# Performance work log

Hardware: AMD Instinct MI355X
Metric: run time of the kernel (lower is better)

The kernel has to match this reference:

```python
import jax, jax.numpy as jnp
import numpy as np

N, H, HD = 512, 8, 128          # n_nodes, n_heads, h feature dim
M0, M1 = 256, 256               # mlp_units
NORM_CONST = 1.0


def setup_inputs() -> dict:
    key = jax.random.key(0)
    ks = jax.random.split(key, 16)
    def w(k, i, o, scale=1.0):
        return jax.random.normal(k, (i, o), jnp.float32) * (scale / np.sqrt(i))
    F = HD + H * H               # h_concat dim = 128 + 64 = 192
    EIN = H + 2 * F              # edge MLP input dim = 8 + 384 = 392
    return {
        "x": jax.random.normal(ks[0], (N, H, 3), jnp.float32),
        "h": jax.random.normal(ks[1], (N, HD), jnp.float32),
        # phi_e: MLP([256,256], silu, activate_final=True)
        "We0": w(ks[2], EIN, M0), "be0": jnp.zeros((M0,), jnp.float32),
        "We1": w(ks[3], M0, M1), "be1": jnp.zeros((M1,), jnp.float32),
        # phi_inf: Linear(1) + sigmoid
        "Winf": w(ks[4], M1, 1), "binf": jnp.zeros((1,), jnp.float32),
        # phi_x: MLP([256,256], silu, activate_final=True) -> Linear(n_heads) (variance-scaled small init)
        "Wx0": w(ks[5], M1, M0), "bx0": jnp.zeros((M0,), jnp.float32),
        "Wx1": w(ks[6], M0, M1), "bx1": jnp.zeros((M1,), jnp.float32),
        "Wxo": w(ks[7], M1, H, scale=0.03), "bxo": jnp.zeros((H,), jnp.float32),
        # phi_h: MLP([256,256], silu, activate_final=False)... note haiku MLP applies
        # activation between layers; final Linear(h_dim) appended in forward.
        "Wh0": w(ks[8], M1 + HD, M0), "bh0": jnp.zeros((M0,), jnp.float32),
        "Wh1": w(ks[9], M0, M1), "bh1": jnp.zeros((M1,), jnp.float32),
        "Who": w(ks[10], M1, HD), "bho": jnp.zeros((HD,), jnp.float32),
    }


def _forward(x, h, We0, be0, We1, be1, Winf, binf, Wx0, bx0, Wx1, bx1,
             Wxo, bxo, Wh0, bh0, Wh1, bh1, Who, bho):
    n, nh = x.shape[0], x.shape[1]
    silu = jax.nn.silu
    off = 1.0 - jnp.eye(n, dtype=x.dtype)                  # off-diagonal node mask
    # per-node head-pair squared distances -> [N, H*H] (diag naturally 0)
    dh = x[:, :, None, :] - x[:, None, :, :]               # [N,H,H,3]
    sqh = jnp.sum(dh * dh, axis=-1).reshape(n, nh * nh)
    hc = jnp.concatenate([h, sqh], axis=-1)                # [N, F]
    # all-pairs node diffs per head: dn[i,j,h] = x[j,h] - x[i,h]
    dn = x[None] - x[:, None]                              # [N,N,H,3]
    sqn = jnp.sum(dn * dn, axis=-1)                        # [N,N,H]
    F = hc.shape[-1]
    hc_j = jnp.broadcast_to(hc[None], (n, n, F))           # receiver-side: hc[j]
    hc_i = jnp.broadcast_to(hc[:, None], (n, n, F))        # sender-side: hc[i]
    edge_in = jnp.concatenate([sqn, hc_j, hc_i], axis=-1)  # [N,N,H+2F]
    # phi_e (activate_final=True), zero self-edges
    m = silu(silu(edge_in @ We0 + be0) @ We1 + be1) * off[:, :, None]
    # gate + message aggregation
    e = jax.nn.sigmoid(m @ Winf + binf)[..., 0] * off      # [N,N]
    m_i = jnp.einsum('ijd,ij->id', m, e)                   # [N,M1]
    # phi_x multi-head coordinate weights (tanh=False), zero self-edges
    px = (silu(silu(m @ Wx0 + bx0) @ Wx1 + bx1) @ Wxo + bxo) * off[:, :, None]
    # normalize_by_x_norm=True path
    norm = jnp.sqrt(sqn + 1e-8) + NORM_CONST               # [N,N,H]
    ndiff = (dn / norm[..., None]) * off[:, :, None, None]
    shift = jnp.einsum('ijhd,ijh->ihd', ndiff, px) / (n - 1)  # agg='mean'
    x_new = x + shift
    # phi_h with residual
    ph_in = jnp.concatenate([m_i, h], axis=-1)
    h_new = h + silu(silu(ph_in @ Wh0 + bh0) @ Wh1 + bh1) @ Who + bho
    return x_new, h_new


def reference(x, h, We0, be0, We1, be1, Winf, binf, Wx0, bx0, Wx1, bx1,
              Wxo, bxo, Wh0, bh0, Wh1, bh1, Who, bho):
    return _forward(x, h, We0, be0, We1, be1, Winf, binf, Wx0, bx0, Wx1, bx1,
                    Wxo, bxo, Wh0, bh0, Wh1, bh1, Who, bho)
```

## Files before the change

kernel.cpp:

```cpp
#include <hip/hip_runtime.h>
#include <math.h>

#define N_NODES 512
#define NH 8
#define HD 128
#define M 256
#define PITCH 264
#define JTILE 64
#define RPW 16

typedef __bf16 v8bf __attribute__((ext_vector_type(8)));
typedef float f32x4 __attribute__((ext_vector_type(4)));
typedef unsigned short us4v __attribute__((ext_vector_type(4)));

__device__ __forceinline__ float silu_f(float v) {
  return v * __builtin_amdgcn_rcpf(1.f + __expf(-v));
}
__device__ __forceinline__ float sigmoid_f(float v) {
  return __builtin_amdgcn_rcpf(1.f + __expf(-v));
}
__device__ __forceinline__ unsigned short f2bf(float f) {
  unsigned u = __float_as_uint(f);
  u += 0x7fffu + ((u >> 16) & 1u);
  return (unsigned short)(u >> 16);
}
__device__ __forceinline__ unsigned short f2bf_hi(float f) {
  return (unsigned short)((__float_as_uint(f) + 0x8000u) >> 16);
}
__device__ __forceinline__ float bf2f(unsigned short s) {
  return __uint_as_float(((unsigned)s) << 16);
}

__device__ __forceinline__ void gl2lds16(const unsigned short* g, unsigned short* l) {
  __builtin_amdgcn_global_load_lds(
      (const __attribute__((address_space(1))) unsigned int*)g,
      (__attribute__((address_space(3))) unsigned int*)l, 16, 0, 0);
}

__global__ __launch_bounds__(256) void k_pre(
    const float* __restrict__ x, const float* __restrict__ h,
    const float* __restrict__ We0, const float* __restrict__ be0,
    const float* __restrict__ We1, const float* __restrict__ Wx0,
    const float* __restrict__ Wx1, const float* __restrict__ Wxo,
    unsigned short* __restrict__ wsB,
    float* __restrict__ P, float* __restrict__ Q,
    float* __restrict__ mi, float* __restrict__ shift)
{
  const int t = threadIdx.x;
  if (blockIdx.x < 816) {
    const int gid = blockIdx.x * 256 + t;
    if (gid >= 208896) return;
    float val;
    int dst;
    if (gid < 196608) {
      const int layer = gid >> 16, e = gid & 65535;
      const int k = e >> 8, n = e & 255;
      const float* W = (layer == 0) ? We1 : (layer == 1) ? Wx0 : Wx1;
      val = W[e];
      const int kt = k >> 5, w = k & 31, quad = w >> 3, j = w & 7;
      const int nt = n >> 4, lnib = n & 15;
      dst = layer * 65536 + ((kt * 16 + nt) * 64 + quad * 16 + lnib) * 8 + j;
    } else if (gid < 198656) {
      const int e = gid - 196608;
      val = Wxo[e];
      const int k = e >> 3, col = e & 7;
      const int kt = k >> 5, w = k & 31, quad = w >> 3, j = w & 7;
      dst = 196608 + (kt * 64 + quad * 16 + col) * 8 + j;
    } else if (gid < 200704) {
      const int e = gid - 198656;
      val = 0.f;
      const int k = e >> 3, col = e & 7;
      const int kt = k >> 5, w = k & 31, quad = w >> 3, j = w & 7;
      dst = 196608 + (kt * 64 + quad * 16 + col + 8) * 8 + j;
    } else if (gid < 202752) {
      const int e = gid - 200704;
      val = We0[e];
      const int j = e >> 8, n = e & 255, nt = n >> 4, lnib = n & 15;
      dst = 200704 + (nt * 64 + lnib) * 8 + j;
    } else {
      const int e = gid - 202752;
      val = 0.f;
      const int q = 1 + (e >> 11), rem = e & 2047;
      const int j = rem & 7, lnib = (rem >> 3) & 15, nt = rem >> 7;
      dst = 200704 + (nt * 64 + q * 16 + lnib) * 8 + j;
    }
    wsB[dst] = f2bf(val);
    return;
  }
  const int i = blockIdx.x - 816;
  __shared__ float s_x[24];
  __shared__ float s_hc[192];
  mi[i * M + t] = 0.f;
  if (t < 24) { shift[i * 24 + t] = 0.f; s_x[t] = x[i * 24 + t]; }
  __syncthreads();
  if (t < HD) {
    s_hc[t] = h[i * HD + t];
  } else if (t < 192) {
    const int p = t - HD, a = p >> 3, b = p & 7;
    float s = 0.f;
#pragma unroll
    for (int d = 0; d < 3; ++d) {
      const float dx = s_x[a * 3 + d] - s_x[b * 3 + d];
      s = fmaf(dx, dx, s);
    }
    s_hc[t] = s;
  }
  __syncthreads();
  float p = 0.f, q = 0.f;
  for (int k = 0; k < 192; ++k) {
    const float hv = s_hc[k];
    p = fmaf(hv, We0[(8 + k) * M + t], p);
    q = fmaf(hv, We0[(200 + k) * M + t], q);
  }
  P[i * M + t] = p;
  Q[i * M + t] = q + be0[t];
}

__global__ __launch_bounds__(512, 4) void k_edge(
    const float* __restrict__ x,
    const float* __restrict__ P, const float* __restrict__ Q,
    const float* __restrict__ be1,
    const float* __restrict__ Winf, const float* __restrict__ binf,
    const float* __restrict__ bx0, const float* __restrict__ bx1,
    const float* __restrict__ bxo,
    const unsigned short* __restrict__ wsB,
    float* __restrict__ mi_acc, float* __restrict__ shift_acc)
{
  const int i  = blockIdx.x;
  const int j0 = blockIdx.y * JTILE;
  const int t  = threadIdx.x;
  const int lane = t & 63, wave = t >> 6;
  const int lnib = lane & 15, quad = lane >> 4;
  const int rg = wave >> 1, c = wave & 1;
  const int r0 = rg * RPW;
  const int jw = j0 + r0;
  const int cb = c * 128;

  __shared__ __align__(16) unsigned short a_act[JTILE * PITCH];
  __shared__ __align__(16) unsigned short B_buf[2][8192];
  __shared__ __align__(16) float s_sqn[JTILE][8];
  __shared__ __align__(16) unsigned short s_sqnb[JTILE][8];
  __shared__ float s_red[JTILE][2];
  __shared__ float s_e[JTILE];

  auto stage = [&](const unsigned short* __restrict__ Bg, int kt, int which) {
    const unsigned short* src = Bg + kt * 8192 + wave * 1024 + lane * 8;
    unsigned short* dst = &B_buf[which][wave * 1024];
    gl2lds16(src,       dst);
    gl2lds16(src + 512, dst + 512);
  };

#pragma unroll
  for (int kk = 0; kk < 2; ++kk) {
    const int idx = kk * 64 + lane;
    const int r = idx >> 3, hh = idx & 7;
    const int j = jw + r;
    float s = 0.f;
#pragma unroll
    for (int d = 0; d < 3; ++d) {
      const float dx = x[j * 24 + hh * 3 + d] - x[i * 24 + hh * 3 + d];
      s = fmaf(dx, dx, s);
    }
    s_sqn[r0 + r][hh] = s;
    s_sqnb[r0 + r][hh] = f2bf(s);
  }

  stage(wsB, 0, 0);

  const float binf0 = binf[0];

  f32x4 acc[8];

  {
#pragma unroll
    for (int nt = 0; nt < 8; ++nt)
#pragma unroll
      for (int reg = 0; reg < 4; ++reg)
        acc[nt][reg] = P[(jw + quad * 4 + reg) * M + cb + nt * 16 + lnib];
    const v8bf aS = *(const v8bf*)&s_sqnb[r0 + lnib][0];
    const unsigned short* B0 = wsB + 200704;
#pragma unroll
    for (int nt = 0; nt < 8; ++nt) {
      const v8bf bv = *(const v8bf*)&B0[((c * 8 + nt) * 64 + lane) * 8];
      acc[nt] = __builtin_amdgcn_mfma_f32_16x16x32_bf16(aS, bv, acc[nt], 0, 0, 0);
    }
#pragma unroll
    for (int nt = 0; nt < 8; ++nt) {
      const float qv = Q[i * M + cb + nt * 16 + lnib];
#pragma unroll
      for (int reg = 0; reg < 4; ++reg) {
        const int row = r0 + quad * 4 + reg;
        a_act[row * PITCH + cb + nt * 16 + lnib] = f2bf_hi(silu_f(acc[nt][reg] + qv));
      }
    }
  }

  auto run_gemm = [&](const unsigned short* __restrict__ Bg,
                      const unsigned short* __restrict__ Bnext) {
    __syncthreads();
#pragma unroll
    for (int kt = 0; kt < 8; ++kt) {
      if (kt < 7)      stage(Bg, kt + 1, (kt + 1) & 1);
      else if (Bnext)  stage(Bnext, 0, 0);
      const v8bf a0 = *(const v8bf*)&a_act[(r0 + lnib) * PITCH + kt * 32 + quad * 8];
#pragma unroll
      for (int nt = 0; nt < 8; ++nt) {
        const v8bf bv = *(const v8bf*)&B_buf[kt & 1][(c * 8 + nt) * 512 + lane * 8];
        acc[nt] = __builtin_amdgcn_mfma_f32_16x16x32_bf16(a0, bv, acc[nt], 0, 0, 0);
      }
      __syncthreads();
    }
  };

#pragma unroll
  for (int nt = 0; nt < 8; ++nt) {
    const float b = be1[cb + nt * 16 + lnib];
    acc[nt] = (f32x4){b, b, b, b};
  }
  run_gemm(wsB, wsB + 65536);
  {
    float ge[4] = {0.f, 0.f, 0.f, 0.f};
#pragma unroll
    for (int nt = 0; nt < 8; ++nt) {
      const float wfv = Winf[cb + nt * 16 + lnib];
#pragma unroll
      for (int reg = 0; reg < 4; ++reg) {
        float v = silu_f(acc[nt][reg]);
        const int row = r0 + quad * 4 + reg;
        if (j0 + row == i) v = 0.f;
        a_act[row * PITCH + cb + nt * 16 + lnib] = f2bf_hi(v);
        ge[reg] = fmaf(v, wfv, ge[reg]);
      }
    }
#pragma unroll
    for (int reg = 0; reg < 4; ++reg) {
      float g = ge[reg];
      g += __shfl_xor(g, 1);
      g += __shfl_xor(g, 2);
      g += __shfl_xor(g, 4);
      g += __shfl_xor(g, 8);
      if (lnib == 0) s_red[r0 + quad * 4 + reg][c] = g;
    }
  }
  __syncthreads();
  if (t < JTILE) s_e[t] = sigmoid_f(s_red[t][0] + s_red[t][1] + binf0);
  __syncthreads();

  {
    const int ch = cb + lane * 2;
    float m0 = 0.f, m1 = 0.f;
#pragma unroll
    for (int r = 0; r < RPW; ++r) {
      const unsigned mv = *(const unsigned*)&a_act[(r0 + r) * PITCH + ch];
      const float ev = s_e[r0 + r];
      m0 = fmaf(bf2f((unsigned short)(mv & 0xffffu)), ev, m0);
      m1 = fmaf(bf2f((unsigned short)(mv >> 16)), ev, m1);
    }
    atomicAdd(&mi_acc[i * M + ch + 0], m0);
    atomicAdd(&mi_acc[i * M + ch + 1], m1);
  }

#pragma unroll
  for (int nt = 0; nt < 8; ++nt) {
    const float b = bx0[cb + nt * 16 + lnib];
    acc[nt] = (f32x4){b, b, b, b};
  }
  run_gemm(wsB + 65536, wsB + 131072);
#pragma unroll
  for (int nt = 0; nt < 8; ++nt)
#pragma unroll
    for (int reg = 0; reg < 4; ++reg) {
      const int row = r0 + quad * 4 + reg;
      a_act[row * PITCH + cb + nt * 16 + lnib] = f2bf_hi(silu_f(acc[nt][reg]));
    }

#pragma unroll
  for (int nt = 0; nt < 8; ++nt) {
    const float b = bx1[cb + nt * 16 + lnib];
    acc[nt] = (f32x4){b, b, b, b};
  }
  run_gemm(wsB + 131072, nullptr);
#pragma unroll
  for (int nt = 0; nt < 8; ++nt)
#pragma unroll
    for (int reg = 0; reg < 4; ++reg) {
      const int row = r0 + quad * 4 + reg;
      a_act[row * PITCH + cb + nt * 16 + lnib] = f2bf_hi(silu_f(acc[nt][reg]));
    }
  __syncthreads();

  if (c == 0) {
    f32x4 px;
    {
      const float b = (lnib < 8) ? bxo[lnib] : 0.f;
      px = (f32x4){b, b, b, b};
      const unsigned short* B = wsB + 196608;
#pragma unroll
      for (int kt = 0; kt < 8; ++kt) {
        const v8bf a0 = *(const v8bf*)&a_act[(r0 + lnib) * PITCH + kt * 32 + quad * 8];
        const v8bf bv = *(const v8bf*)&B[(kt * 64 + lane) * 8];
        px = __builtin_amdgcn_mfma_f32_16x16x32_bf16(a0, bv, px, 0, 0, 0);
      }
    }
    const int hh = lnib & 7;
    const float xi0 = x[i * 24 + hh * 3 + 0];
    const float xi1 = x[i * 24 + hh * 3 + 1];
    const float xi2 = x[i * 24 + hh * 3 + 2];
    float p0 = 0.f, p1 = 0.f, p2 = 0.f;
#pragma unroll
    for (int reg = 0; reg < 4; ++reg) {
      const int row = r0 + quad * 4 + reg;
      const int jg = j0 + row;
      if (jg != i) {
        const float pxv = px[reg];
        const float sq  = s_sqn[row][hh];
        const float f   = pxv * __builtin_amdgcn_rcpf(sqrtf(sq + 1e-8f) + 1.f);
        p0 = fmaf(x[jg * 24 + hh * 3 + 0] - xi0, f, p0);
        p1 = fmaf(x[jg * 24 + hh * 3 + 1] - xi1, f, p1);
        p2 = fmaf(x[jg * 24 + hh * 3 + 2] - xi2, f, p2);
      }
    }
    p0 += __shfl_xor(p0, 16); p0 += __shfl_xor(p0, 32);
    p1 += __shfl_xor(p1, 16); p1 += __shfl_xor(p1, 32);
    p2 += __shfl_xor(p2, 16); p2 += __shfl_xor(p2, 32);
    if (lane < 8) {
      atomicAdd(&shift_acc[i * 24 + hh * 3 + 0], p0);
      atomicAdd(&shift_acc[i * 24 + hh * 3 + 1], p1);
      atomicAdd(&shift_acc[i * 24 + hh * 3 + 2], p2);
    }
  }
}

__global__ __launch_bounds__(256) void k_hout(
    const float* __restrict__ x, const float* __restrict__ shift,
    const float* __restrict__ h, const float* __restrict__ mi,
    const float* __restrict__ Wh0, const float* __restrict__ bh0,
    const float* __restrict__ Wh1, const float* __restrict__ bh1,
    const float* __restrict__ Who, const float* __restrict__ bho,
    float* __restrict__ out_x, float* __restrict__ out_h)
{
  const int i = blockIdx.x, t = threadIdx.x;
  __shared__ float s_in[M + HD];
  __shared__ float s_b[M];
  if (t < 24) out_x[i * 24 + t] = x[i * 24 + t] + shift[i * 24 + t] * (1.f / 511.f);
  s_in[t] = mi[i * M + t];
  if (t < HD) s_in[M + t] = h[i * HD + t];
  __syncthreads();
  float acc = bh0[t];
  for (int k = 0; k < M + HD; ++k) acc = fmaf(s_in[k], Wh0[k * M + t], acc);
  s_b[t] = silu_f(acc);
  __syncthreads();
  float acc2 = bh1[t];
  for (int k = 0; k < M; ++k) acc2 = fmaf(s_b[k], Wh1[k * M + t], acc2);
  const float a1v = silu_f(acc2);
  __syncthreads();
  s_in[t] = a1v;
  __syncthreads();
  if (t < HD) {
    float o = bho[t];
    for (int k = 0; k < M; ++k) o = fmaf(s_in[k], Who[k * HD + t], o);
    out_h[i * HD + t] = h[i * HD + t] + o;
  }
}

extern "C" void kernel_launch(void* const* d_in, const int* in_sizes, int n_in,
                              void* d_out, int out_size, void* d_ws, size_t ws_size,
                              hipStream_t stream)
{
  const float* x    = (const float*)d_in[0];
  const float* h    = (const float*)d_in[1];
  const float* We0  = (const float*)d_in[2];
  const float* be0  = (const float*)d_in[3];
  const float* We1  = (const float*)d_in[4];
  const float* be1  = (const float*)d_in[5];
  const float* Winf = (const float*)d_in[6];
  const float* binf = (const float*)d_in[7];
  const float* Wx0  = (const float*)d_in[8];
  const float* bx0  = (const float*)d_in[9];
  const float* Wx1  = (const float*)d_in[10];
  const float* bx1  = (const float*)d_in[11];
  const float* Wxo  = (const float*)d_in[12];
  const float* bxo  = (const float*)d_in[13];
  const float* Wh0  = (const float*)d_in[14];
  const float* bh0  = (const float*)d_in[15];
  const float* Wh1  = (const float*)d_in[16];
  const float* bh1  = (const float*)d_in[17];
  const float* Who  = (const float*)d_in[18];
  const float* bho  = (const float*)d_in[19];

  float* out_x = (float*)d_out;
  float* out_h = out_x + N_NODES * NH * 3;

  float* ws    = (float*)d_ws;
  float* mi    = ws;
  float* shift = ws + 131072;
  float* P     = ws + 143360;
  float* Q     = ws + 274432;
  unsigned short* wsB = (unsigned short*)(ws + 405504);

  k_pre<<<816 + N_NODES, 256, 0, stream>>>(
      x, h, We0, be0, We1, Wx0, Wx1, Wxo, wsB, P, Q, mi, shift);
  k_edge<<<dim3(N_NODES, N_NODES / JTILE), 512, 0, stream>>>(
      x, P, Q, be1, Winf, binf, bx0, bx1, bxo, wsB, mi, shift);
  k_hout<<<N_NODES, 256, 0, stream>>>(
      x, shift, h, mi, Wh0, bh0, Wh1, bh1, Who, bho, out_x, out_h);
}
```

Measured before the change: 307.8 us.

## Retile edge MLP to 4 waves with 4x4 MFMA tiles and swapped operands

The edge kernel moves from 8 waves of 16 rows by 128 columns to 4 waves that each own 64 columns across all 64 edges. Each wave now runs a 4x4 grid of MFMA tiles, so every loaded A and B fragment is reused four times. Operands are swapped so each lane's accumulator holds four consecutive channels, which allows vectorized bias/P/Q loads and packed bf16 stores via v_cvt_pk_bf16. The tradeoff is higher register pressure from 16 accumulators per lane and fewer waves per block, which may lower occupancy and latency hiding.

```diff
diff --git a/kernel.cpp b/kernel.cpp
--- a/kernel.cpp
+++ b/kernel.cpp
@@ -7,11 +7,10 @@
 #define M 256
 #define PITCH 264
 #define JTILE 64
-#define RPW 16
 
 typedef __bf16 v8bf __attribute__((ext_vector_type(8)));
 typedef float f32x4 __attribute__((ext_vector_type(4)));
-typedef unsigned short us4v __attribute__((ext_vector_type(4)));
+typedef unsigned uint2v __attribute__((ext_vector_type(2)));
 
 __device__ __forceinline__ float silu_f(float v) {
   return v * __builtin_amdgcn_rcpf(1.f + __expf(-v));
@@ -24,11 +23,13 @@
   u += 0x7fffu + ((u >> 16) & 1u);
   return (unsigned short)(u >> 16);
 }
-__device__ __forceinline__ unsigned short f2bf_hi(float f) {
-  return (unsigned short)((__float_as_uint(f) + 0x8000u) >> 16);
-}
 __device__ __forceinline__ float bf2f(unsigned short s) {
   return __uint_as_float(((unsigned)s) << 16);
+}
+__device__ __forceinline__ unsigned cvt_pk_bf16(float lo, float hi) {
+  unsigned r;
+  asm("v_cvt_pk_bf16_f32 %0, %1, %2" : "=v"(r) : "v"(lo), "v"(hi));
+  return r;
 }
 
 __device__ __forceinline__ void gl2lds16(const unsigned short* g, unsigned short* l) {
@@ -116,7 +117,7 @@
   Q[i * M + t] = q + be0[t];
 }
 
-__global__ __launch_bounds__(512, 4) void k_edge(
+__global__ __launch_bounds__(256, 2) void k_edge(
     const float* __restrict__ x,
     const float* __restrict__ P, const float* __restrict__ Q,
     const float* __restrict__ be1,
@@ -129,68 +130,77 @@
   const int i  = blockIdx.x;
   const int j0 = blockIdx.y * JTILE;
   const int t  = threadIdx.x;
-  const int lane = t & 63, wave = t >> 6;
+  const int lane = t & 63, wq = t >> 6;
   const int lnib = lane & 15, quad = lane >> 4;
-  const int rg = wave >> 1, c = wave & 1;
-  const int r0 = rg * RPW;
-  const int jw = j0 + r0;
-  const int cb = c * 128;
+  const int cb = wq * 64;
 
   __shared__ __align__(16) unsigned short a_act[JTILE * PITCH];
   __shared__ __align__(16) unsigned short B_buf[2][8192];
   __shared__ __align__(16) float s_sqn[JTILE][8];
   __shared__ __align__(16) unsigned short s_sqnb[JTILE][8];
-  __shared__ float s_red[JTILE][2];
+  __shared__ float s_red[JTILE][4];
   __shared__ float s_e[JTILE];
 
   auto stage = [&](const unsigned short* __restrict__ Bg, int kt, int which) {
-    const unsigned short* src = Bg + kt * 8192 + wave * 1024 + lane * 8;
-    unsigned short* dst = &B_buf[which][wave * 1024];
-    gl2lds16(src,       dst);
-    gl2lds16(src + 512, dst + 512);
+    const unsigned short* src = Bg + kt * 8192 + wq * 2048 + lane * 8;
+    unsigned short* dst = &B_buf[which][wq * 2048];
+    gl2lds16(src,        dst);
+    gl2lds16(src + 512,  dst + 512);
+    gl2lds16(src + 1024, dst + 1024);
+    gl2lds16(src + 1536, dst + 1536);
   };
 
 #pragma unroll
   for (int kk = 0; kk < 2; ++kk) {
-    const int idx = kk * 64 + lane;
+    const int idx = kk * 256 + t;
     const int r = idx >> 3, hh = idx & 7;
-    const int j = jw + r;
+    const int j = j0 + r;
     float s = 0.f;
 #pragma unroll
     for (int d = 0; d < 3; ++d) {
       const float dx = x[j * 24 + hh * 3 + d] - x[i * 24 + hh * 3 + d];
       s = fmaf(dx, dx, s);
     }
-    s_sqn[r0 + r][hh] = s;
-    s_sqnb[r0 + r][hh] = f2bf(s);
+    s_sqn[r][hh] = s;
+    s_sqnb[r][hh] = f2bf(s);
   }
 
   stage(wsB, 0, 0);
-
   const float binf0 = binf[0];
-
-  f32x4 acc[8];
+  __syncthreads();
+
+  f32x4 acc[4][4];
 
   {
 #pragma unroll
-    for (int nt = 0; nt < 8; ++nt)
-#pragma unroll
-      for (int reg = 0; reg < 4; ++reg)
-        acc[nt][reg] = P[(jw + quad * 4 + reg) * M + cb + nt * 16 + lnib];
-    const v8bf aS = *(const v8bf*)&s_sqnb[r0 + lnib][0];
-    const unsigned short* B0 = wsB + 200704;
-#pragma unroll
-    for (int nt = 0; nt < 8; ++nt) {
-      const v8bf bv = *(const v8bf*)&B0[((c * 8 + nt) * 64 + lane) * 8];
-      acc[nt] = __builtin_amdgcn_mfma_f32_16x16x32_bf16(aS, bv, acc[nt], 0, 0, 0);
-    }
-#pragma unroll
-    for (int nt = 0; nt < 8; ++nt) {
-      const float qv = Q[i * M + cb + nt * 16 + lnib];
-#pragma unroll
-      for (int reg = 0; reg < 4; ++reg) {
-        const int row = r0 + quad * 4 + reg;
-        a_act[row * PITCH + cb + nt * 16 + lnib] = f2bf_hi(silu_f(acc[nt][reg] + qv));
+    for (int ct = 0; ct < 4; ++ct)
+#pragma unroll
+      for (int et = 0; et < 4; ++et)
+        acc[ct][et] = *(const f32x4*)&P[(j0 + et * 16 + lnib) * M + cb + ct * 16 + quad * 4];
+    const unsigned short* W0 = wsB + 200704;
+    v8bf wf[4], af[4];
+#pragma unroll
+    for (int ct = 0; ct < 4; ++ct)
+      wf[ct] = *(const v8bf*)&W0[((wq * 4 + ct) * 64 + lane) * 8];
+#pragma unroll
+    for (int et = 0; et < 4; ++et)
+      af[et] = *(const v8bf*)&s_sqnb[et * 16 + lnib][0];
+#pragma unroll
+    for (int ct = 0; ct < 4; ++ct)
+#pragma unroll
+      for (int et = 0; et < 4; ++et)
+        acc[ct][et] = __builtin_amdgcn_mfma_f32_16x16x32_bf16(wf[ct], af[et], acc[ct][et], 0, 0, 0);
+#pragma unroll
+    for (int ct = 0; ct < 4; ++ct) {
+      const f32x4 qv = *(const f32x4*)&Q[i * M + cb + ct * 16 + quad * 4];
+#pragma unroll
+      for (int et = 0; et < 4; ++et) {
+        const int row = et * 16 + lnib;
+        const unsigned w0 = cvt_pk_bf16(silu_f(acc[ct][et][0] + qv[0]),
+                                        silu_f(acc[ct][et][1] + qv[1]));
+        const unsigned w1 = cvt_pk_bf16(silu_f(acc[ct][et][2] + qv[2]),
+                                        silu_f(acc[ct][et][3] + qv[3]));
+        *(uint2v*)&a_act[row * PITCH + cb + ct * 16 + quad * 4] = (uint2v){w0, w1};
       }
     }
   }
@@ -202,131 +212,161 @@
     for (int kt = 0; kt < 8; ++kt) {
       if (kt < 7)      stage(Bg, kt + 1, (kt + 1) & 1);
       else if (Bnext)  stage(Bnext, 0, 0);
-      const v8bf a0 = *(const v8bf*)&a_act[(r0 + lnib) * PITCH + kt * 32 + quad * 8];
-#pragma unroll
-      for (int nt = 0; nt < 8; ++nt) {
-        const v8bf bv = *(const v8bf*)&B_buf[kt & 1][(c * 8 + nt) * 512 + lane * 8];
-        acc[nt] = __builtin_amdgcn_mfma_f32_16x16x32_bf16(a0, bv, acc[nt], 0, 0, 0);
-      }
+      v8bf wf[4], af[4];
+#pragma unroll
+      for (int ct = 0; ct < 4; ++ct)
+        wf[ct] = *(const v8bf*)&B_buf[kt & 1][(wq * 4 + ct) * 512 + lane * 8];
+#pragma unroll
+      for (int et = 0; et < 4; ++et)
+        af[et] = *(const v8bf*)&a_act[(et * 16 + lnib) * PITCH + kt * 32 + quad * 8];
+#pragma unroll
+      for (int ct = 0; ct < 4; ++ct)
+#pragma unroll
+        for (int et = 0; et < 4; ++et)
+          acc[ct][et] = __builtin_amdgcn_mfma_f32_16x16x32_bf16(wf[ct], af[et], acc[ct][et], 0, 0, 0);
       __syncthreads();
     }
   };
 
 #pragma unroll
-  for (int nt = 0; nt < 8; ++nt) {
-    const float b = be1[cb + nt * 16 + lnib];
-    acc[nt] = (f32x4){b, b, b, b};
+  for (int ct = 0; ct < 4; ++ct) {
+    const f32x4 b = *(const f32x4*)&be1[cb + ct * 16 + quad * 4];
+#pragma unroll
+    for (int et = 0; et < 4; ++et) acc[ct][et] = b;
   }
   run_gemm(wsB, wsB + 65536);
   {
     float ge[4] = {0.f, 0.f, 0.f, 0.f};
 #pragma unroll
-    for (int nt = 0; nt < 8; ++nt) {
-      const float wfv = Winf[cb + nt * 16 + lnib];
-#pragma unroll
-      for (int reg = 0; reg < 4; ++reg) {
-        float v = silu_f(acc[nt][reg]);
-        const int row = r0 + quad * 4 + reg;
-        if (j0 + row == i) v = 0.f;
-        a_act[row * PITCH + cb + nt * 16 + lnib] = f2bf_hi(v);
-        ge[reg] = fmaf(v, wfv, ge[reg]);
+    for (int ct = 0; ct < 4; ++ct) {
+      const f32x4 wv = *(const f32x4*)&Winf[cb + ct * 16 + quad * 4];
+#pragma unroll
+      for (int et = 0; et < 4; ++et) {
+        const int row = et * 16 + lnib;
+        const bool dz = (j0 + row == i);
+        const float v0 = dz ? 0.f : silu_f(acc[ct][et][0]);
+        const float v1 = dz ? 0.f : silu_f(acc[ct][et][1]);
+        const float v2 = dz ? 0.f : silu_f(acc[ct][et][2]);
+        const float v3 = dz ? 0.f : silu_f(acc[ct][et][3]);
+        ge[et] = fmaf(v0, wv[0], ge[et]);
+        ge[et] = fmaf(v1, wv[1], ge[et]);
+        ge[et] = fmaf(v2, wv[2], ge[et]);
+        ge[et] = fmaf(v3, wv[3], ge[et]);
+        *(uint2v*)&a_act[row * PITCH + cb + ct * 16 + quad * 4] =
+            (uint2v){cvt_pk_bf16(v0, v1), cvt_pk_bf16(v2, v3)};
       }
     }
 #pragma unroll
-    for (int reg = 0; reg < 4; ++reg) {
-      float g = ge[reg];
-      g += __shfl_xor(g, 1);
-      g += __shfl_xor(g, 2);
-      g += __shfl_xor(g, 4);
-      g += __shfl_xor(g, 8);
-      if (lnib == 0) s_red[r0 + quad * 4 + reg][c] = g;
-    }
-  }
-  __syncthreads();
-  if (t < JTILE) s_e[t] = sigmoid_f(s_red[t][0] + s_red[t][1] + binf0);
+    for (int et = 0; et < 4; ++et) {
+      float g = ge[et];
+      g += __shfl_xor(g, 16);
+      g += __shfl_xor(g, 32);
+      if (quad == 0) s_red[et * 16 + lnib][wq] = g;
+    }
+  }
+  __syncthreads();
+  if (t < JTILE)
+    s_e[t] = sigmoid_f(s_red[t][0] + s_red[t][1] + s_red[t][2] + s_red[t][3] + binf0);
   __syncthreads();
 
   {
-    const int ch = cb + lane * 2;
-    float m0 = 0.f, m1 = 0.f;
-#pragma unroll
-    for (int r = 0; r < RPW; ++r) {
-      const unsigned mv = *(const unsigned*)&a_act[(r0 + r) * PITCH + ch];
+    const int r0 = wq * 16;
+    float m0 = 0.f, m1 = 0.f, m2 = 0.f, m3 = 0.f;
+#pragma unroll
+    for (int r = 0; r < 16; ++r) {
       const float ev = s_e[r0 + r];
-      m0 = fmaf(bf2f((unsigned short)(mv & 0xffffu)), ev, m0);
-      m1 = fmaf(bf2f((unsigned short)(mv >> 16)), ev, m1);
-    }
-    atomicAdd(&mi_acc[i * M + ch + 0], m0);
-    atomicAdd(&mi_acc[i * M + ch + 1], m1);
-  }
-
-#pragma unroll
-  for (int nt = 0; nt < 8; ++nt) {
-    const float b = bx0[cb + nt * 16 + lnib];
-    acc[nt] = (f32x4){b, b, b, b};
+      const unsigned pa = *(const unsigned*)&a_act[(r0 + r) * PITCH + lane * 2];
+      const unsigned pb = *(const unsigned*)&a_act[(r0 + r) * PITCH + 128 + lane * 2];
+      m0 = fmaf(bf2f((unsigned short)(pa & 0xffffu)), ev, m0);
+      m1 = fmaf(bf2f((unsigned short)(pa >> 16)), ev, m1);
+      m2 = fmaf(bf2f((unsigned short)(pb & 0xffffu)), ev, m2);
+      m3 = fmaf(bf2f((unsigned short)(pb >> 16)), ev, m3);
+    }
+    atomicAdd(&mi_acc[i * M + lane * 2 + 0], m0);
+    atomicAdd(&mi_acc[i * M + lane * 2 + 1], m1);
+    atomicAdd(&mi_acc[i * M + 128 + lane * 2 + 0], m2);
+    atomicAdd(&mi_acc[i * M + 128 + lane * 2 + 1], m3);
+  }
+
+#pragma unroll
+  for (int ct = 0; ct < 4; ++ct) {
+    const f32x4 b = *(const f32x4*)&bx0[cb + ct * 16 + quad * 4];
+#pragma unroll
+    for (int et = 0; et < 4; ++et) acc[ct][et] = b;
   }
   run_gemm(wsB + 65536, wsB + 131072);
 #pragma unroll
-  for (int nt = 0; nt < 8; ++nt)
-#pragma unroll
-    for (int reg = 0; reg < 4; ++reg) {
-      const int row = r0 + quad * 4 + reg;
-      a_act[row * PITCH + cb + nt * 16 + lnib] = f2bf_hi(silu_f(acc[nt][reg]));
-    }
-
-#pragma unroll
-  for (int nt = 0; nt < 8; ++nt) {
-    const float b = bx1[cb + nt * 16 + lnib];
-    acc[nt] = (f32x4){b, b, b, b};
+  for (int ct = 0; ct < 4; ++ct)
+#pragma unroll
+    for (int et = 0; et < 4; ++et) {
+      const int row = et * 16 + lnib;
+      const unsigned w0 = cvt_pk_bf16(silu_f(acc[ct][et][0]), silu_f(acc[ct][et][1]));
+      const unsigned w1 = cvt_pk_bf16(silu_f(acc[ct][et][2]), silu_f(acc[ct][et][3]));
+      *(uint2v*)&a_act[row * PITCH + cb + ct * 16 + quad * 4] = (uint2v){w0, w1};
+    }
+
+#pragma unroll
+  for (int ct = 0; ct < 4; ++ct) {
+    const f32x4 b = *(const f32x4*)&bx1[cb + ct * 16 + quad * 4];
+#pragma unroll
+    for (int et = 0; et < 4; ++et) acc[ct][et] = b;
   }
   run_gemm(wsB + 131072, nullptr);
 #pragma unroll
-  for (int nt = 0; nt < 8; ++nt)
-#pragma unroll
-    for (int reg = 0; reg < 4; ++reg) {
-      const int row = r0 + quad * 4 + reg;
-      a_act[row * PITCH + cb + nt * 16 + lnib] = f2bf_hi(silu_f(acc[nt][reg]));
-    }
-  __syncthreads();
-
-  if (c == 0) {
+  for (int ct = 0; ct < 4; ++ct)
+#pragma unroll
+    for (int et = 0; et < 4; ++et) {
+      const int row = et * 16 + lnib;
+      const unsigned w0 = cvt_pk_bf16(silu_f(acc[ct][et][0]), silu_f(acc[ct][et][1]));
+      const unsigned w1 = cvt_pk_bf16(silu_f(acc[ct][et][2]), silu_f(acc[ct][et][3]));
+      *(uint2v*)&a_act[row * PITCH + cb + ct * 16 + quad * 4] = (uint2v){w0, w1};
+    }
+  __syncthreads();
+
+  {
+    const int e0 = wq * 16;
     f32x4 px;
-    {
-      const float b = (lnib < 8) ? bxo[lnib] : 0.f;
-      px = (f32x4){b, b, b, b};
-      const unsigned short* B = wsB + 196608;
-#pragma unroll
-      for (int kt = 0; kt < 8; ++kt) {
-        const v8bf a0 = *(const v8bf*)&a_act[(r0 + lnib) * PITCH + kt * 32 + quad * 8];
-        const v8bf bv = *(const v8bf*)&B[(kt * 64 + lane) * 8];
-        px = __builtin_amdgcn_mfma_f32_16x16x32_bf16(a0, bv, px, 0, 0, 0);
+    if (quad < 2) px = *(const f32x4*)&bxo[quad * 4];
+    else          px = (f32x4){0.f, 0.f, 0.f, 0.f};
+    const unsigned short* Bx = wsB + 196608;
+#pragma unroll
+    for (int kt = 0; kt < 8; ++kt) {
+      const v8bf af = *(const v8bf*)&a_act[(e0 + lnib) * PITCH + kt * 32 + quad * 8];
+      const v8bf wf = *(const v8bf*)&Bx[(kt * 64 + lane) * 8];
+      px = __builtin_amdgcn_mfma_f32_16x16x32_bf16(wf, af, px, 0, 0, 0);
+    }
+    const int jg = j0 + e0 + lnib;
+    float c0[4], c1[4], c2[4];
+#pragma unroll
+    for (int r = 0; r < 4; ++r) { c0[r] = 0.f; c1[r] = 0.f; c2[r] = 0.f; }
+    if (quad < 2 && jg != i) {
+#pragma unroll
+      for (int r = 0; r < 4; ++r) {
+        const int hh = quad * 4 + r;
+        const float sq = s_sqn[e0 + lnib][hh];
+        const float f  = px[r] * __builtin_amdgcn_rcpf(sqrtf(sq + 1e-8f) + 1.f);
+        c0[r] = (x[jg * 24 + hh * 3 + 0] - x[i * 24 + hh * 3 + 0]) * f;
+        c1[r] = (x[jg * 24 + hh * 3 + 1] - x[i * 24 + hh * 3 + 1]) * f;
+        c2[r] = (x[jg * 24 + hh * 3 + 2] - x[i * 24 + hh * 3 + 2]) * f;
       }
     }
-    const int hh = lnib & 7;
-    const float xi0 = x[i * 24 + hh * 3 + 0];
-    const float xi1 = x[i * 24 + hh * 3 + 1];
-    const float xi2 = x[i * 24 + hh * 3 + 2];
-    float p0 = 0.f, p1 = 0.f, p2 = 0.f;
-#pragma unroll
-    for (int reg = 0; reg < 4; ++reg) {
-      const int row = r0 + quad * 4 + reg;
-      const int jg = j0 + row;
-      if (jg != i) {
-        const float pxv = px[reg];
-        const float sq  = s_sqn[row][hh];
-        const float f   = pxv * __builtin_amdgcn_rcpf(sqrtf(sq + 1e-8f) + 1.f);
-        p0 = fmaf(x[jg * 24 + hh * 3 + 0] - xi0, f, p0);
-        p1 = fmaf(x[jg * 24 + hh * 3 + 1] - xi1, f, p1);
-        p2 = fmaf(x[jg * 24 + hh * 3 + 2] - xi2, f, p2);
+#pragma unroll
+    for (int r = 0; r < 4; ++r) {
+#pragma unroll
+      for (int s = 1; s <= 8; s <<= 1) {
+        c0[r] += __shfl_xor(c0[r], s);
+        c1[r] += __shfl_xor(c1[r], s);
+        c2[r] += __shfl_xor(c2[r], s);
       }
     }
-    p0 += __shfl_xor(p0, 16); p0 += __shfl_xor(p0, 32);
-    p1 += __shfl_xor(p1, 16); p1 += __shfl_xor(p1, 32);
-    p2 += __shfl_xor(p2, 16); p2 += __shfl_xor(p2, 32);
-    if (lane < 8) {
-      atomicAdd(&shift_acc[i * 24 + hh * 3 + 0], p0);
-      atomicAdd(&shift_acc[i * 24 + hh * 3 + 1], p1);
-      atomicAdd(&shift_acc[i * 24 + hh * 3 + 2], p2);
+    if (lnib == 0 && quad < 2) {
+#pragma unroll
+      for (int r = 0; r < 4; ++r) {
+        const int hh = quad * 4 + r;
+        atomicAdd(&shift_acc[i * 24 + hh * 3 + 0], c0[r]);
+        atomicAdd(&shift_acc[i * 24 + hh * 3 + 1], c1[r]);
+        atomicAdd(&shift_acc[i * 24 + hh * 3 + 2], c2[r]);
+      }
     }
   }
 }
@@ -400,7 +440,7 @@
 
   k_pre<<<816 + N_NODES, 256, 0, stream>>>(
       x, h, We0, be0, We1, Wx0, Wx1, Wxo, wsB, P, Q, mi, shift);
-  k_edge<<<dim3(N_NODES, N_NODES / JTILE), 512, 0, stream>>>(
+  k_edge<<<dim3(N_NODES, N_NODES / JTILE), 256, 0, stream>>>(
       x, P, Q, be1, Winf, binf, bx0, bx1, bxo, wsB, mi, shift);
   k_hout<<<N_NODES, 256, 0, stream>>>(
       x, shift, h, mi, Wh0, bh0, Wh1, bh1, Who, bho, out_x, out_h);
```

Result: slower. 332.4 us (+8.0%).
